# Kernel optimization log

Hardware: AMD Instinct MI355X
Metric: run time of the kernel (lower is better)

The kernel has to match this reference:

```python
import jax, jax.numpy as jnp
import numpy as np
from itertools import combinations_with_replacement

IN_FEATURES = 128
ORDER = 3
BIAS = True
WEIGHT_DIVISOR = 100.0
BATCH = 256


def _make_comb_idx():
    n_feat = IN_FEATURES + (1 if BIAS else 0)  # 129
    idx = np.array(list(combinations_with_replacement(range(n_feat), ORDER)), dtype=np.int32)
    return jnp.asarray(idx)  # [num_combinations, ORDER] = [366145, 3]


def setup_inputs() -> dict:
    key = jax.random.key(0)
    kx, kw = jax.random.split(key)
    x = jax.random.normal(kx, (BATCH, IN_FEATURES), dtype=jnp.float32)
    comb_idx = _make_comb_idx()
    num_weights = comb_idx.shape[0]
    weight = jax.random.uniform(kw, (num_weights,), dtype=jnp.float32) / WEIGHT_DIVISOR
    return {"x": x, "weight": weight, "comb_idx": comb_idx}


def reference(x, weight, comb_idx):
    # Prepend bias column of ones: xb [B, in_features+1]
    ones = jnp.ones((x.shape[0], 1), dtype=x.dtype)
    xb = jnp.concatenate([ones, x], axis=1)
    # Gather per-combination features: [B, num_combinations, ORDER]
    gathered = xb[:, comb_idx]
    # Monomial products: [B, num_combinations]
    colx = jnp.prod(gathered, axis=2)
    # Weighted sum -> [B, 1]; activation is identity
    return colx @ weight[:, None]
```

## Files before the change

kernel.cpp:

```cpp
#include <hip/hip_runtime.h>


#define NF      129
#define NCOMB   366145
#define NPAIR   8385
#define NT      4
#define NCHUNK  132
#define NKS     5

typedef short bf16x8 __attribute__((ext_vector_type(8)));
typedef float f32x4  __attribute__((ext_vector_type(4)));

static __device__ inline unsigned short f2bf(float f) {
    union { float f; unsigned u; } v; v.f = f;
    return (unsigned short)((v.u + 0x7fffu + ((v.u >> 16) & 1u)) >> 16);
}

__global__ __launch_bounds__(256, 3) void honu_fused(const float* __restrict__ x,
                                                     const float* __restrict__ w,
                                                     float* __restrict__ out) {
    __shared__ float  xf[64 * NF];
    __shared__ bf16x8 wls[NT * NKS * 64];
    __shared__ int2   dec[64];

    const int tid  = threadIdx.x;
    const int lane = tid & 63;
    const int wv   = tid >> 6;
    const int bx   = blockIdx.x;
    const int by   = blockIdx.y;

    {
        const int r = tid >> 2, q = tid & 3;
        const float4* xr = (const float4*)(x + (size_t)(by * 64 + r) * 128);
        #pragma unroll
        for (int t = 0; t < 8; ++t) {
            const int c4 = q + 4 * t;
            const float4 v = xr[c4];
            float* d = &xf[r * NF + 1 + 4 * c4];
            d[0] = v.x; d[1] = v.y; d[2] = v.z; d[3] = v.w;
        }
        if (tid < 64) xf[tid * NF] = 1.0f;
    }

    if (tid < 64) {
        const int p = bx * 64 + tid;
        int i0 = 0, i1 = 0, mb = 0;
        if (p < NPAIR) {
            i0 = (int)((259.0f - sqrtf((float)(67081 - 8 * p))) * 0.5f);
            i0 = i0 < 0 ? 0 : (i0 > 128 ? 128 : i0);
            while (i0 < 128 && ((i0 + 1) * (258 - i0)) / 2 <= p) ++i0;
            while (i0 > 0   && (i0 * (259 - i0)) / 2      >  p) --i0;
            i1 = i0 + (p - (i0 * (259 - i0)) / 2);
            const int n0 = NF - i0, n1 = NF - i1;
            mb = NCOMB - (n0 * (n0 + 1) * (n0 + 2)) / 6
                       + ((n0 * (n0 + 1)) >> 1) - ((n1 * (n1 + 1)) >> 1);
        }
        dec[tid] = make_int2(i0 | (i1 << 16), mb);
    }
    __syncthreads();

    #pragma unroll
    for (int it = 0; it < NT * NKS * 64 / 256; ++it) {
        const int item = tid + it * 256;
        const int lx = item & 63;
        const int fs = item >> 6;
        const int s  = fs % NKS, nt = fs / NKS;
        const int pl = nt * 16 + (lx & 15);
        const int kb = s * 32 + (lx >> 4) * 8;
        const int2 pd = dec[pl];
        const int i1 = pd.x >> 16, mb = pd.y;
        const bool pok = (bx * 64 + pl) < NPAIR;
        bf16x8 v = (bf16x8)0;
        if (pok && kb >= i1 && kb + 7 <= 128) {
            const float* src = w + mb + (kb - i1);
            #pragma unroll
            for (int j = 0; j < 8; ++j) v[j] = (short)f2bf(src[j]);
        } else if (pok && kb + 7 >= i1 && kb <= 128) {
            #pragma unroll
            for (int j = 0; j < 8; ++j) {
                const int k = kb + j;
                if (k >= i1 && k <= 128) v[j] = (short)f2bf(w[mb + k - i1]);
            }
        }
        wls[fs * 64 + lx] = v;
    }
    __syncthreads();

    const int am = wv * 16 + (lane & 15);
    const int aq = (lane >> 4) * 8;
    bf16x8 a[NKS];
    #pragma unroll
    for (int s = 0; s < NKS; ++s) {
        #pragma unroll
        for (int j = 0; j < 8; ++j) {
            const int k = s * 32 + aq + j;
            a[s][j] = (k <= 128) ? (short)f2bf(xf[am * NF + k]) : (short)0;
        }
    }

    const int lr0 = wv * 16 + (lane >> 4) * 4;
    const float* r0 = &xf[lr0 * NF];
    float o0 = 0.f, o1 = 0.f, o2 = 0.f, o3 = 0.f;

    #pragma unroll
    for (int nt = 0; nt < NT; ++nt) {
        f32x4 acc = {0.f, 0.f, 0.f, 0.f};
        #pragma unroll
        for (int s = 0; s < NKS; ++s)
            acc = __builtin_amdgcn_mfma_f32_16x16x32_bf16(
                      a[s], wls[(nt * NKS + s) * 64 + lane], acc, 0, 0, 0);
        const int2 pd = dec[nt * 16 + (lane & 15)];
        const int i0 = pd.x & 0xffff, i1 = pd.x >> 16;
        o0 = fmaf(acc[0], r0[i0]          * r0[i1],          o0);
        o1 = fmaf(acc[1], r0[NF + i0]     * r0[NF + i1],     o1);
        o2 = fmaf(acc[2], r0[2 * NF + i0] * r0[2 * NF + i1], o2);
        o3 = fmaf(acc[3], r0[3 * NF + i0] * r0[3 * NF + i1], o3);
    }

    #pragma unroll
    for (int msk = 1; msk < 16; msk <<= 1) {
        o0 += __shfl_xor(o0, msk);
        o1 += __shfl_xor(o1, msk);
        o2 += __shfl_xor(o2, msk);
        o3 += __shfl_xor(o3, msk);
    }
    if ((lane & 15) == 0) {
        float* po = out + by * 64 + lr0;
        atomicAdd(po + 0, o0);
        atomicAdd(po + 1, o1);
        atomicAdd(po + 2, o2);
        atomicAdd(po + 3, o3);
    }
}

extern "C" void kernel_launch(void* const* d_in, const int* in_sizes, int n_in,
                              void* d_out, int out_size, void* d_ws, size_t ws_size,
                              hipStream_t stream) {
    const float* x      = (const float*)d_in[0];
    const float* weight = (const float*)d_in[1];
    float* out = (float*)d_out;

    honu_fused<<<dim3(NCHUNK, 4), 256, 0, stream>>>(x, weight, out);
}
```

Measured before the change: 79.05 us.

## Stage contiguous weight slice in LDS and skip zero k-steps in MFMA loop

Each block now loads its contiguous slice of the weight vector into LDS as bf16 with a coalesced strided loop, replacing the per-fragment scattered global gathers. The B fragments are then built from LDS with per-element bounds checks that point to a zero sentinel. The MFMA k-loop starts at the smallest k-step any pair in the 16-lane tile needs, which skips all-zero blocks. In exchange, operand assembly now does 8 scalar LDS reads per MFMA, and the loop trip count is data-dependent, which limits unrolling.

```diff
diff --git a/kernel.cpp b/kernel.cpp
--- a/kernel.cpp
+++ b/kernel.cpp
@@ -7,6 +7,8 @@
 #define NT      4
 #define NCHUNK  132
 #define NKS     5
+#define WRAWSZ  6304
+#define ZS      6303
 
 typedef short bf16x8 __attribute__((ext_vector_type(8)));
 typedef float f32x4  __attribute__((ext_vector_type(4)));
@@ -16,18 +18,39 @@
     return (unsigned short)((v.u + 0x7fffu + ((v.u >> 16) & 1u)) >> 16);
 }
 
+static __device__ inline void dpair(int p, int& i0, int& i1) {
+    int t = (int)((259.0f - sqrtf((float)(67081 - 8 * p))) * 0.5f);
+    t = t < 0 ? 0 : (t > 128 ? 128 : t);
+    while (t < 128 && ((t + 1) * (258 - t)) / 2 <= p) ++t;
+    while (t > 0   && (t * (259 - t)) / 2      >  p) --t;
+    i0 = t; i1 = t + (p - (t * (259 - t)) / 2);
+}
+
+static __device__ inline int mbase(int i0, int i1) {
+    const int n0 = NF - i0, n1 = NF - i1;
+    return NCOMB - (n0 * (n0 + 1) * (n0 + 2)) / 6
+                 + ((n0 * (n0 + 1)) >> 1) - ((n1 * (n1 + 1)) >> 1);
+}
+
 __global__ __launch_bounds__(256, 3) void honu_fused(const float* __restrict__ x,
                                                      const float* __restrict__ w,
                                                      float* __restrict__ out) {
-    __shared__ float  xf[64 * NF];
-    __shared__ bf16x8 wls[NT * NKS * 64];
-    __shared__ int2   dec[64];
+    __shared__ float          xf[64 * NF];
+    __shared__ unsigned short wraw[WRAWSZ];
+    __shared__ int2           dec[64];
 
     const int tid  = threadIdx.x;
     const int lane = tid & 63;
     const int wv   = tid >> 6;
     const int bx   = blockIdx.x;
     const int by   = blockIdx.y;
+
+    const int p0 = bx * 64;
+    int a0, a1; dpair(p0, a0, a1);
+    const int mstart = mbase(a0, a1);
+    int mend = NCOMB;
+    if (p0 + 64 < NPAIR) { int b0, b1; dpair(p0 + 64, b0, b1); mend = mbase(b0, b1); }
+    const int L = mend - mstart;
 
     {
         const int r = tid >> 2, q = tid & 3;
@@ -42,47 +65,17 @@
         if (tid < 64) xf[tid * NF] = 1.0f;
     }
 
+    for (int i = tid; i < L; i += 256) wraw[i] = f2bf(w[mstart + i]);
+    if (tid == 0) wraw[ZS] = 0;
+
     if (tid < 64) {
-        const int p = bx * 64 + tid;
-        int i0 = 0, i1 = 0, mb = 0;
+        const int p = p0 + tid;
+        int i0 = 0, i1 = 129, bo = 0;
         if (p < NPAIR) {
-            i0 = (int)((259.0f - sqrtf((float)(67081 - 8 * p))) * 0.5f);
-            i0 = i0 < 0 ? 0 : (i0 > 128 ? 128 : i0);
-            while (i0 < 128 && ((i0 + 1) * (258 - i0)) / 2 <= p) ++i0;
-            while (i0 > 0   && (i0 * (259 - i0)) / 2      >  p) --i0;
-            i1 = i0 + (p - (i0 * (259 - i0)) / 2);
-            const int n0 = NF - i0, n1 = NF - i1;
-            mb = NCOMB - (n0 * (n0 + 1) * (n0 + 2)) / 6
-                       + ((n0 * (n0 + 1)) >> 1) - ((n1 * (n1 + 1)) >> 1);
+            dpair(p, i0, i1);
+            bo = (mbase(i0, i1) - mstart) - i1;
         }
-        dec[tid] = make_int2(i0 | (i1 << 16), mb);
-    }
-    __syncthreads();
-
-    #pragma unroll
-    for (int it = 0; it < NT * NKS * 64 / 256; ++it) {
-        const int item = tid + it * 256;
-        const int lx = item & 63;
-        const int fs = item >> 6;
-        const int s  = fs % NKS, nt = fs / NKS;
-        const int pl = nt * 16 + (lx & 15);
-        const int kb = s * 32 + (lx >> 4) * 8;
-        const int2 pd = dec[pl];
-        const int i1 = pd.x >> 16, mb = pd.y;
-        const bool pok = (bx * 64 + pl) < NPAIR;
-        bf16x8 v = (bf16x8)0;
-        if (pok && kb >= i1 && kb + 7 <= 128) {
-            const float* src = w + mb + (kb - i1);
-            #pragma unroll
-            for (int j = 0; j < 8; ++j) v[j] = (short)f2bf(src[j]);
-        } else if (pok && kb + 7 >= i1 && kb <= 128) {
-            #pragma unroll
-            for (int j = 0; j < 8; ++j) {
-                const int k = kb + j;
-                if (k >= i1 && k <= 128) v[j] = (short)f2bf(w[mb + k - i1]);
-            }
-        }
-        wls[fs * 64 + lx] = v;
+        dec[tid] = make_int2(i0 | (i1 << 16), bo);
     }
     __syncthreads();
 
@@ -104,13 +97,32 @@
 
     #pragma unroll
     for (int nt = 0; nt < NT; ++nt) {
+        const int2 pd = dec[nt * 16 + (lane & 15)];
+        const int i1f = pd.x >> 16;
+        const int bo  = pd.y;
+
+        int mn = i1f;
+        mn = min(mn, __shfl_xor(mn, 1));
+        mn = min(mn, __shfl_xor(mn, 2));
+        mn = min(mn, __shfl_xor(mn, 4));
+        mn = min(mn, __shfl_xor(mn, 8));
+        const int smin = mn >> 5;
+
         f32x4 acc = {0.f, 0.f, 0.f, 0.f};
-        #pragma unroll
-        for (int s = 0; s < NKS; ++s)
-            acc = __builtin_amdgcn_mfma_f32_16x16x32_bf16(
-                      a[s], wls[(nt * NKS + s) * 64 + lane], acc, 0, 0, 0);
-        const int2 pd = dec[nt * 16 + (lane & 15)];
-        const int i0 = pd.x & 0xffff, i1 = pd.x >> 16;
+        for (int s = smin; s < NKS; ++s) {
+            const int kb = s * 32 + aq;
+            bf16x8 bf;
+            #pragma unroll
+            for (int j = 0; j < 8; ++j) {
+                const int k  = kb + j;
+                const int ad = (k >= i1f && k <= 128) ? bo + k : ZS;
+                bf[j] = (short)wraw[ad];
+            }
+            acc = __builtin_amdgcn_mfma_f32_16x16x32_bf16(a[s], bf, acc, 0, 0, 0);
+        }
+
+        const int i0 = pd.x & 0xffff;
+        const int i1 = i1f > 128 ? 128 : i1f;
         o0 = fmaf(acc[0], r0[i0]          * r0[i1],          o0);
         o1 = fmaf(acc[1], r0[NF + i0]     * r0[NF + i1],     o1);
         o2 = fmaf(acc[2], r0[2 * NF + i0] * r0[2 * NF + i1], o2);
```

New measurement: 111.5 us. 41.1% more time.

## Cut K to 128 with an FP32 tail term, streamline weight staging

Applied to the files above, without the earlier changes.

Shrinks the MFMA K dimension from 160 to 128 by dropping the last feature column (k=128) from the bf16 GEMM. Its contribution is added back in FP32 using a per-pair weight loaded during pair decoding. Weight staging is simplified to one pair/segment per item with clamped unconditional loads and a cheaper bf16 pack, and the A-fragment conversion now runs before the second barrier so a barrier is dropped. This removes 20% of the MFMAs and the staging loop work, but it changes the rounding mode (round-half-up instead of round-to-nearest-even) and relies on a sentinel i1 value for invalid pairs.

```diff
diff --git a/kernel.cpp b/kernel.cpp
--- a/kernel.cpp
+++ b/kernel.cpp
@@ -6,14 +6,30 @@
 #define NPAIR   8385
 #define NT      4
 #define NCHUNK  132
-#define NKS     5
+#define NKS     4
 
 typedef short bf16x8 __attribute__((ext_vector_type(8)));
 typedef float f32x4  __attribute__((ext_vector_type(4)));
 
-static __device__ inline unsigned short f2bf(float f) {
-    union { float f; unsigned u; } v; v.f = f;
-    return (unsigned short)((v.u + 0x7fffu + ((v.u >> 16) & 1u)) >> 16);
+union i4b8 { int4 i; bf16x8 b; };
+
+static __device__ inline unsigned bfpack2(float lo, float hi) {
+    union { float f; unsigned u; } a, b; a.f = lo; b.f = hi;
+    return ((b.u + 0x8000u) & 0xffff0000u) | ((a.u + 0x8000u) >> 16);
+}
+
+static __device__ inline void dpair(int p, int& i0, int& i1) {
+    int t = (int)((259.0f - sqrtf((float)(67081 - 8 * p))) * 0.5f);
+    t = t < 0 ? 0 : (t > 128 ? 128 : t);
+    while (t < 128 && ((t + 1) * (258 - t)) / 2 <= p) ++t;
+    while (t > 0   && (t * (259 - t)) / 2      >  p) --t;
+    i0 = t; i1 = t + (p - (t * (259 - t)) / 2);
+}
+
+static __device__ inline int mbase(int i0, int i1) {
+    const int n0 = NF - i0, n1 = NF - i1;
+    return NCOMB - (n0 * (n0 + 1) * (n0 + 2)) / 6
+                 + ((n0 * (n0 + 1)) >> 1) - ((n1 * (n1 + 1)) >> 1);
 }
 
 __global__ __launch_bounds__(256, 3) void honu_fused(const float* __restrict__ x,
@@ -21,7 +37,7 @@
                                                      float* __restrict__ out) {
     __shared__ float  xf[64 * NF];
     __shared__ bf16x8 wls[NT * NKS * 64];
-    __shared__ int2   dec[64];
+    __shared__ int4   dec[64];
 
     const int tid  = threadIdx.x;
     const int lane = tid & 63;
@@ -44,59 +60,60 @@
 
     if (tid < 64) {
         const int p = bx * 64 + tid;
-        int i0 = 0, i1 = 0, mb = 0;
+        int i0 = 0, i1 = 200, mb = 0; unsigned wl = 0;
         if (p < NPAIR) {
-            i0 = (int)((259.0f - sqrtf((float)(67081 - 8 * p))) * 0.5f);
-            i0 = i0 < 0 ? 0 : (i0 > 128 ? 128 : i0);
-            while (i0 < 128 && ((i0 + 1) * (258 - i0)) / 2 <= p) ++i0;
-            while (i0 > 0   && (i0 * (259 - i0)) / 2      >  p) --i0;
-            i1 = i0 + (p - (i0 * (259 - i0)) / 2);
-            const int n0 = NF - i0, n1 = NF - i1;
-            mb = NCOMB - (n0 * (n0 + 1) * (n0 + 2)) / 6
-                       + ((n0 * (n0 + 1)) >> 1) - ((n1 * (n1 + 1)) >> 1);
+            dpair(p, i0, i1);
+            mb = mbase(i0, i1);
+            union { float f; unsigned u; } c; c.f = w[mb + 128 - i1];
+            wl = c.u;
         }
-        dec[tid] = make_int2(i0 | (i1 << 16), mb);
+        dec[tid] = make_int4(i0 | (i1 << 16), mb, (int)wl, 0);
     }
     __syncthreads();
 
     #pragma unroll
-    for (int it = 0; it < NT * NKS * 64 / 256; ++it) {
+    for (int it = 0; it < 4; ++it) {
         const int item = tid + it * 256;
-        const int lx = item & 63;
-        const int fs = item >> 6;
-        const int s  = fs % NKS, nt = fs / NKS;
-        const int pl = nt * 16 + (lx & 15);
-        const int kb = s * 32 + (lx >> 4) * 8;
-        const int2 pd = dec[pl];
-        const int i1 = pd.x >> 16, mb = pd.y;
-        const bool pok = (bx * 64 + pl) < NPAIR;
-        bf16x8 v = (bf16x8)0;
-        if (pok && kb >= i1 && kb + 7 <= 128) {
-            const float* src = w + mb + (kb - i1);
-            #pragma unroll
-            for (int j = 0; j < 8; ++j) v[j] = (short)f2bf(src[j]);
-        } else if (pok && kb + 7 >= i1 && kb <= 128) {
+        const int pl = item >> 4, r = item & 15;
+        const int4 pd = dec[pl];
+        const int i1 = pd.x >> 16;
+        const int mb = pd.y;
+        const int k0 = r * 8;
+        int4 vout = make_int4(0, 0, 0, 0);
+        if (k0 + 7 >= i1) {
+            float f[8];
             #pragma unroll
             for (int j = 0; j < 8; ++j) {
-                const int k = kb + j;
-                if (k >= i1 && k <= 128) v[j] = (short)f2bf(w[mb + k - i1]);
+                const int k = k0 + j;
+                int off = k - i1; off = off < 0 ? 0 : off;
+                const float t = w[mb + off];
+                f[j] = (k >= i1) ? t : 0.0f;
             }
+            vout.x = (int)bfpack2(f[0], f[1]);
+            vout.y = (int)bfpack2(f[2], f[3]);
+            vout.z = (int)bfpack2(f[4], f[5]);
+            vout.w = (int)bfpack2(f[6], f[7]);
         }
-        wls[fs * 64 + lx] = v;
+        const int nt = pl >> 4, s = r >> 2;
+        const int slane = ((r & 3) << 4) | (pl & 15);
+        ((int4*)wls)[(nt * NKS + s) * 64 + slane] = vout;
     }
-    __syncthreads();
 
     const int am = wv * 16 + (lane & 15);
     const int aq = (lane >> 4) * 8;
+    const float* xa = &xf[am * NF + aq];
     bf16x8 a[NKS];
     #pragma unroll
     for (int s = 0; s < NKS; ++s) {
-        #pragma unroll
-        for (int j = 0; j < 8; ++j) {
-            const int k = s * 32 + aq + j;
-            a[s][j] = (k <= 128) ? (short)f2bf(xf[am * NF + k]) : (short)0;
-        }
+        const float* p = xa + s * 32;
+        i4b8 av;
+        av.i.x = (int)bfpack2(p[0], p[1]);
+        av.i.y = (int)bfpack2(p[2], p[3]);
+        av.i.z = (int)bfpack2(p[4], p[5]);
+        av.i.w = (int)bfpack2(p[6], p[7]);
+        a[s] = av.b;
     }
+    __syncthreads();
 
     const int lr0 = wv * 16 + (lane >> 4) * 4;
     const float* r0 = &xf[lr0 * NF];
@@ -109,12 +126,16 @@
         for (int s = 0; s < NKS; ++s)
             acc = __builtin_amdgcn_mfma_f32_16x16x32_bf16(
                       a[s], wls[(nt * NKS + s) * 64 + lane], acc, 0, 0, 0);
-        const int2 pd = dec[nt * 16 + (lane & 15)];
-        const int i0 = pd.x & 0xffff, i1 = pd.x >> 16;
-        o0 = fmaf(acc[0], r0[i0]          * r0[i1],          o0);
-        o1 = fmaf(acc[1], r0[NF + i0]     * r0[NF + i1],     o1);
-        o2 = fmaf(acc[2], r0[2 * NF + i0] * r0[2 * NF + i1], o2);
-        o3 = fmaf(acc[3], r0[3 * NF + i0] * r0[3 * NF + i1], o3);
+
+        const int4 pd = dec[nt * 16 + (lane & 15)];
+        const int i0 = pd.x & 0xffff;
+        int i1 = pd.x >> 16; if (i1 > 128) i1 = 0;
+        union { int i; float f; } wc; wc.i = pd.z;
+        const float wl = wc.f;
+        o0 = fmaf(acc[0] + r0[128]          * wl, r0[i0]          * r0[i1],          o0);
+        o1 = fmaf(acc[1] + r0[NF + 128]     * wl, r0[NF + i0]     * r0[NF + i1],     o1);
+        o2 = fmaf(acc[2] + r0[2 * NF + 128] * wl, r0[2 * NF + i0] * r0[2 * NF + i1], o2);
+        o3 = fmaf(acc[3] + r0[3 * NF + 128] * wl, r0[3 * NF + i0] * r0[3 * NF + i1], o3);
     }
 
     #pragma unroll
```

Result: faster. 76.82 us (-2.8%).
